# Kernel tuning notes

Hardware: AMD Instinct MI355X
Metric: run time of the kernel (lower is better)

## Reference

```python
import math
import jax, jax.numpy as jnp
import numpy as np

GROUPS = 32
EPS = 1e-5


def group_norm(x, w, b):
    # x: [B, C, H, W]
    B, C, H, W = x.shape
    xg = x.reshape(B, GROUPS, C // GROUPS, H, W)
    mean = xg.mean(axis=(2, 3, 4), keepdims=True)
    var = xg.var(axis=(2, 3, 4), keepdims=True)
    xg = (xg - mean) * jax.lax.rsqrt(var + EPS)
    x = xg.reshape(B, C, H, W)
    return x * w[None, :, None, None] + b[None, :, None, None]


def setup_inputs() -> dict:
    key = jax.random.key(0)
    ks = jax.random.split(key, 4)
    B, C, H, W = 16, 512, 32, 32
    x = jax.random.normal(ks[0], (B, C, H, W), dtype=jnp.float32)
    norm_w = jnp.ones((C,), dtype=jnp.float32)
    norm_b = jnp.zeros((C,), dtype=jnp.float32)
    qkv_w = jax.random.normal(ks[1], (3 * C, C), dtype=jnp.float32) / math.sqrt(C)
    qkv_b = jnp.zeros((3 * C,), dtype=jnp.float32)
    proj_w = jax.random.normal(ks[2], (C, C), dtype=jnp.float32) / math.sqrt(C)
    proj_b = jnp.zeros((C,), dtype=jnp.float32)
    return {"x": x, "norm_w": norm_w, "norm_b": norm_b,
            "qkv_w": qkv_w, "qkv_b": qkv_b,
            "proj_w": proj_w, "proj_b": proj_b}


def reference(x, norm_w, norm_b, qkv_w, qkv_b, proj_w, proj_b):
    B, C, H, W = x.shape
    xn = group_norm(x, norm_w, norm_b)
    # 1x1 conv == channel matmul: [B,3C,H,W]
    qkv = jnp.einsum('oc,bchw->bohw', qkv_w, xn) + qkv_b[None, :, None, None]
    q, k, v = jnp.split(qkv, 3, axis=1)
    q = q.reshape(B, C, H * W).transpose(0, 2, 1)  # [B, HW, C]
    k = k.reshape(B, C, H * W)                     # [B, C, HW]
    v = v.reshape(B, C, H * W).transpose(0, 2, 1)  # [B, HW, C]
    attn = jax.nn.softmax(jnp.einsum('bnc,bcm->bnm', q, k) / math.sqrt(C), axis=-1)
    h = jnp.einsum('bnm,bmc->bnc', attn, v)        # [B, HW, C]
    h = h.transpose(0, 2, 1).reshape(B, C, H, W)
    out = jnp.einsum('oc,bchw->bohw', proj_w, h) + proj_b[None, :, None, None]
    return out + x
```

## Files before the change

### kernel.cpp

```cpp
#include <hip/hip_runtime.h>

#define GLD16(gp, lp) __builtin_amdgcn_global_load_lds( \
    (const __attribute__((address_space(1))) void*)(gp), \
    (__attribute__((address_space(3))) void*)(lp), 16, 0, 0)

typedef __attribute__((ext_vector_type(8))) short bf16x8;
typedef __attribute__((ext_vector_type(4))) float f32x4;

__device__ __forceinline__ short f2bf(float f) {
    union { float f; unsigned u; } x; x.f = f;
    unsigned r = x.u + 0x7fffu + ((x.u >> 16) & 1u);
    return (short)(r >> 16);
}
__device__ __forceinline__ float bf2f(short s) {
    union { unsigned u; float f; } x;
    x.u = ((unsigned)(unsigned short)s) << 16;
    return x.f;
}
__device__ __forceinline__ int xcd_swz(int id, int n) {
    return (id & 7) * (n >> 3) + (id >> 3);
}

__global__ __launch_bounds__(256) void prep(
    const float* __restrict__ qkv_w, const float* __restrict__ proj_w,
    short* __restrict__ wq, short* __restrict__ wp,
    const float* __restrict__ x, float* __restrict__ mean, float* __restrict__ rstd)
{
    if (blockIdx.x < 1024) {
        int idx = blockIdx.x * 256 + threadIdx.x;
        const int NQ4 = (1536 * 512) / 4;
        float4 f; short4 s;
        if (idx < NQ4) {
            f = ((const float4*)qkv_w)[idx];
            s.x = f2bf(f.x); s.y = f2bf(f.y); s.z = f2bf(f.z); s.w = f2bf(f.w);
            ((short4*)wq)[idx] = s;
        } else {
            int j = idx - NQ4;
            f = ((const float4*)proj_w)[j];
            s.x = f2bf(f.x); s.y = f2bf(f.y); s.z = f2bf(f.z); s.w = f2bf(f.w);
            ((short4*)wp)[j] = s;
        }
    } else {
        int bg = blockIdx.x - 1024;
        const float4* p = (const float4*)(x + (size_t)bg * 16384);
        float s = 0.f, ss = 0.f;
        for (int i = threadIdx.x; i < 4096; i += 256) {
            float4 v = p[i];
            s  += v.x + v.y + v.z + v.w;
            ss += v.x * v.x + v.y * v.y + v.z * v.z + v.w * v.w;
        }
        #pragma unroll
        for (int o = 32; o > 0; o >>= 1) {
            s  += __shfl_down(s, o);
            ss += __shfl_down(ss, o);
        }
        __shared__ float ls[4], lss[4];
        int wave = threadIdx.x >> 6;
        if ((threadIdx.x & 63) == 0) { ls[wave] = s; lss[wave] = ss; }
        __syncthreads();
        if (threadIdx.x == 0) {
            s  = ls[0] + ls[1] + ls[2] + ls[3];
            ss = lss[0] + lss[1] + lss[2] + lss[3];
            float m = s * (1.f / 16384.f);
            float var = ss * (1.f / 16384.f) - m * m;
            mean[bg] = m;
            rstd[bg] = rsqrtf(var + 1e-5f);
        }
    }
}

__global__ __launch_bounds__(256) void gn_apply_t(
    const float* __restrict__ x, const float* __restrict__ w, const float* __restrict__ bb,
    const float* __restrict__ mean, const float* __restrict__ rstd,
    short* __restrict__ xnT)
{
    __shared__ short tile[64][65];
    int b = blockIdx.z, cblk = blockIdx.y, nblk = blockIdx.x;
    int t = threadIdx.x;
    int nl = t & 63;
    int cb = t >> 6;
    #pragma unroll
    for (int i = 0; i < 16; ++i) {
        int cl = cb * 16 + i;
        int cg = cblk * 64 + cl;
        int bgid = b * 32 + (cg >> 4);
        float sc = rstd[bgid] * w[cg];
        float sh = bb[cg] - mean[bgid] * sc;
        float xv = x[((size_t)(b * 512 + cg)) * 1024 + nblk * 64 + nl];
        tile[cl][nl] = f2bf(xv * sc + sh);
    }
    __syncthreads();
    int ng = t >> 4;
    int c4 = (t & 15) * 4;
    #pragma unroll
    for (int p = 0; p < 4; ++p) {
        int nl2 = p * 16 + ng;
        short4 sv;
        sv.x = tile[c4 + 0][nl2];
        sv.y = tile[c4 + 1][nl2];
        sv.z = tile[c4 + 2][nl2];
        sv.w = tile[c4 + 3][nl2];
        *(short4*)&xnT[((size_t)(b * 1024 + nblk * 64 + nl2)) * 512 + cblk * 64 + c4] = sv;
    }
}

template<int NT>
__device__ __forceinline__ void gemm256_8p(
    const short* __restrict__ A, const short* __restrict__ B,
    const int lda, const int ldb, short* lds, f32x4 acc[8][4])
{
    const int tid  = threadIdx.x;
    const int lane = tid & 63;
    const int wave = tid >> 6;
    const int wm = wave >> 2;
    const int wn = wave & 3;
    const int fr = lane & 15;
    const int fk = lane >> 4;

    const short* pa[2]; const short* pb[2]; int la[2], lb[2];
    #pragma unroll
    for (int i = 0; i < 2; ++i) {
        int cid = i * 512 + tid;
        int row = cid >> 2, sl = cid & 3;
        int csw = sl ^ ((row >> 1) & 3);
        pa[i] = A + (size_t)row * lda + csw * 8;
        pb[i] = B + (size_t)row * ldb + csw * 8;
        la[i] = cid * 8;
        lb[i] = 8192 + cid * 8;
    }

    #pragma unroll
    for (int i = 0; i < 2; ++i) GLD16(pa[i],      lds + la[i]);
    #pragma unroll
    for (int i = 0; i < 2; ++i) GLD16(pb[i],      lds + lb[i]);
    #pragma unroll
    for (int i = 0; i < 2; ++i) GLD16(pa[i] + 32, lds + 16384 + la[i]);
    #pragma unroll
    for (int i = 0; i < 2; ++i) GLD16(pb[i] + 32, lds + 16384 + lb[i]);
    asm volatile("s_waitcnt vmcnt(4)" ::: "memory");
    asm volatile("s_barrier" ::: "memory");

    const int arow0 = wm * 128 + fr;
    const int brow0 = wn * 64 + fr;

    int base = 0, sbase = 32768, kst = 64;
    for (int t = 0; t < NT; ++t) {
        const short* lA = lds + base;
        const short* lB = lds + base + 8192;
        const bool pre = (t + 2 < NT);

        if (pre) {
            GLD16(pa[0] + kst, lds + sbase + la[0]);
            GLD16(pa[1] + kst, lds + sbase + la[1]);
        }
        bf16x8 af[8], bf0[2];
        #pragma unroll
        for (int m = 0; m < 8; ++m) {
            int R = arow0 + m * 16;
            af[m] = *(const bf16x8*)&lA[R * 32 + ((fk ^ ((R >> 1) & 3)) << 3)];
        }
        #pragma unroll
        for (int n = 0; n < 2; ++n) {
            int R = brow0 + n * 16;
            bf0[n] = *(const bf16x8*)&lB[R * 32 + ((fk ^ ((R >> 1) & 3)) << 3)];
        }
        asm volatile("s_barrier" ::: "memory");
        __builtin_amdgcn_s_setprio(1);
        #pragma unroll
        for (int m = 0; m < 8; ++m)
            #pragma unroll
            for (int n = 0; n < 2; ++n)
                acc[m][n] = __builtin_amdgcn_mfma_f32_16x16x32_bf16(af[m], bf0[n], acc[m][n], 0, 0, 0);
        __builtin_amdgcn_s_setprio(0);

        if (pre) {
            GLD16(pb[0] + kst, lds + sbase + lb[0]);
            GLD16(pb[1] + kst, lds + sbase + lb[1]);
        }
        bf16x8 bf1[2];
        #pragma unroll
        for (int n = 0; n < 2; ++n) {
            int R = brow0 + (n + 2) * 16;
            bf1[n] = *(const bf16x8*)&lB[R * 32 + ((fk ^ ((R >> 1) & 3)) << 3)];
        }
        asm volatile("s_barrier" ::: "memory");
        __builtin_amdgcn_s_setprio(1);
        #pragma unroll
        for (int m = 0; m < 8; ++m)
            #pragma unroll
            for (int n = 0; n < 2; ++n)
                acc[m][n + 2] = __builtin_amdgcn_mfma_f32_16x16x32_bf16(af[m], bf1[n], acc[m][n + 2], 0, 0, 0);
        __builtin_amdgcn_s_setprio(0);

        if (pre)                 asm volatile("s_waitcnt vmcnt(4)" ::: "memory");
        else if (t + 1 < NT)     asm volatile("s_waitcnt vmcnt(0)" ::: "memory");
        asm volatile("s_barrier" ::: "memory");
        __builtin_amdgcn_sched_barrier(0);
        base  = (base  == 32768) ? 0 : base  + 16384;
        sbase = (sbase == 32768) ? 0 : sbase + 16384;
        kst += 32;
    }
}

template<int NT>
__device__ __forceinline__ void gemm128x256(
    const short* __restrict__ A, const short* __restrict__ B,
    const int lda, const int ldb, short* lds, f32x4 acc[4][4])
{
    const int tid  = threadIdx.x;
    const int lane = tid & 63;
    const int wave = tid >> 6;
    const int wm = wave >> 2;
    const int wn = wave & 3;
    const int fr = lane & 15;
    const int fk = lane >> 4;

    const short* pa; int la;
    {
        int row = tid >> 2, sl = tid & 3;
        int csw = sl ^ ((row >> 1) & 3);
        pa = A + (size_t)row * lda + csw * 8;
        la = tid * 8;
    }
    const short* pb[2]; int lb[2];
    #pragma unroll
    for (int i = 0; i < 2; ++i) {
        int cid = i * 512 + tid;
        int row = cid >> 2, sl = cid & 3;
        int csw = sl ^ ((row >> 1) & 3);
        pb[i] = B + (size_t)row * ldb + csw * 8;
        lb[i] = 4096 + cid * 8;
    }

    GLD16(pa, lds + la);
    #pragma unroll
    for (int i = 0; i < 2; ++i) GLD16(pb[i], lds + lb[i]);
    GLD16(pa + 32, lds + 12288 + la);
    #pragma unroll
    for (int i = 0; i < 2; ++i) GLD16(pb[i] + 32, lds + 12288 + lb[i]);
    asm volatile("s_waitcnt vmcnt(3)" ::: "memory");
    asm volatile("s_barrier" ::: "memory");

    const int arow0 = wm * 64 + fr;
    const int brow0 = wn * 64 + fr;

    int base = 0, sbase = 24576, kst = 64;
    for (int t = 0; t < NT; ++t) {
        const short* lA = lds + base;
        const short* lB = lds + base + 4096;
        const bool pre = (t + 2 < NT);

        if (pre) GLD16(pa + kst, lds + sbase + la);
        bf16x8 af[4], bf0[2];
        #pragma unroll
        for (int m = 0; m < 4; ++m) {
            int R = arow0 + m * 16;
            af[m] = *(const bf16x8*)&lA[R * 32 + ((fk ^ ((R >> 1) & 3)) << 3)];
        }
        #pragma unroll
        for (int n = 0; n < 2; ++n) {
            int R = brow0 + n * 16;
            bf0[n] = *(const bf16x8*)&lB[R * 32 + ((fk ^ ((R >> 1) & 3)) << 3)];
        }
        asm volatile("s_barrier" ::: "memory");
        __builtin_amdgcn_s_setprio(1);
        #pragma unroll
        for (int m = 0; m < 4; ++m)
            #pragma unroll
            for (int n = 0; n < 2; ++n)
                acc[m][n] = __builtin_amdgcn_mfma_f32_16x16x32_bf16(af[m], bf0[n], acc[m][n], 0, 0, 0);
        __builtin_amdgcn_s_setprio(0);

        if (pre) {
            GLD16(pb[0] + kst, lds + sbase + lb[0]);
            GLD16(pb[1] + kst, lds + sbase + lb[1]);
        }
        bf16x8 bf1[2];
        #pragma unroll
        for (int n = 0; n < 2; ++n) {
            int R = brow0 + (n + 2) * 16;
            bf1[n] = *(const bf16x8*)&lB[R * 32 + ((fk ^ ((R >> 1) & 3)) << 3)];
        }
        asm volatile("s_barrier" ::: "memory");
        __builtin_amdgcn_s_setprio(1);
        #pragma unroll
        for (int m = 0; m < 4; ++m)
            #pragma unroll
            for (int n = 0; n < 2; ++n)
                acc[m][n + 2] = __builtin_amdgcn_mfma_f32_16x16x32_bf16(af[m], bf1[n], acc[m][n + 2], 0, 0, 0);
        __builtin_amdgcn_s_setprio(0);

        if (pre)                 asm volatile("s_waitcnt vmcnt(3)" ::: "memory");
        else if (t + 1 < NT)     asm volatile("s_waitcnt vmcnt(0)" ::: "memory");
        asm volatile("s_barrier" ::: "memory");
        __builtin_amdgcn_sched_barrier(0);
        base  = (base  == 24576) ? 0 : base  + 12288;
        sbase = (sbase == 24576) ? 0 : sbase + 12288;
        kst += 32;
    }
}

#define EPI_IDX8() \
    const int lane = threadIdx.x & 63; \
    const int wave = threadIdx.x >> 6; \
    const int wm = wave >> 2; \
    const int wn = wave & 3; \
    const int fq = lane >> 4; \
    const int fcol = lane & 15;

__global__ __launch_bounds__(512, 2) void qkv_gemm(
    const short* __restrict__ wq, const float* __restrict__ qkv_b,
    const short* __restrict__ xnT,
    short* __restrict__ qT, short* __restrict__ kT, short* __restrict__ vv)
{
    __shared__ short lds[49152];
    int wg = xcd_swz(blockIdx.x, 384);
    const int bm = wg % 6, bn = wg / 6;
    const short* A  = wq + (size_t)bm * 256 * 512;
    const short* Bb = xnT + (size_t)bn * 256 * 512;
    f32x4 acc[8][4];
    #pragma unroll
    for (int m = 0; m < 8; ++m)
        #pragma unroll
        for (int n = 0; n < 4; ++n) acc[m][n] = (f32x4){0.f, 0.f, 0.f, 0.f};
    gemm256_8p<16>(A, Bb, 512, 512, lds, acc);

    EPI_IDX8();
    const int region = bm >> 1;
    const float qscale = 0.04419417382415922f;

    #pragma unroll
    for (int m = 0; m < 8; ++m) {
        int o0 = bm * 256 + wm * 128 + m * 16 + fq * 4;
        float4 bias = *(const float4*)&qkv_b[o0];
        float bb4[4] = {bias.x, bias.y, bias.z, bias.w};
        #pragma unroll
        for (int n = 0; n < 4; ++n) {
            int cf = bn * 256 + wn * 64 + n * 16 + fcol;
            int b = cf >> 10, col = cf & 1023;
            f32x4 a = acc[m][n];
            if (region == 0) {
                short4 sv;
                sv.x = f2bf((a[0] + bb4[0]) * qscale);
                sv.y = f2bf((a[1] + bb4[1]) * qscale);
                sv.z = f2bf((a[2] + bb4[2]) * qscale);
                sv.w = f2bf((a[3] + bb4[3]) * qscale);
                *(short4*)&qT[((size_t)(b * 1024 + col)) * 512 + o0] = sv;
            } else if (region == 1) {
                short4 sv;
                sv.x = f2bf(a[0] + bb4[0]);
                sv.y = f2bf(a[1] + bb4[1]);
                sv.z = f2bf(a[2] + bb4[2]);
                sv.w = f2bf(a[3] + bb4[3]);
                *(short4*)&kT[((size_t)(b * 1024 + col)) * 512 + (o0 - 512)] = sv;
            } else {
                #pragma unroll
                for (int r = 0; r < 4; ++r)
                    vv[((size_t)(b * 512 + (o0 - 1024 + r))) * 1024 + col] = f2bf(a[r] + bb4[r]);
            }
        }
    }
}

__global__ __launch_bounds__(512, 2) void s_gemm(
    const short* __restrict__ kT, const short* __restrict__ qT,
    short* __restrict__ S, float* __restrict__ rowsum)
{
    __shared__ short lds[49152];
    int wg = xcd_swz(blockIdx.x, 256);
    const int bn = wg & 3, bm = (wg >> 2) & 3, b = wg >> 4;
    const short* A  = kT + ((size_t)b * 1024 + bm * 256) * 512;
    const short* Bb = qT + ((size_t)b * 1024 + bn * 256) * 512;
    f32x4 acc[8][4];
    #pragma unroll
    for (int m = 0; m < 8; ++m)
        #pragma unroll
        for (int n = 0; n < 4; ++n) acc[m][n] = (f32x4){0.f, 0.f, 0.f, 0.f};
    gemm256_8p<16>(A, Bb, 512, 512, lds, acc);

    EPI_IDX8();
    float rs[4] = {0.f, 0.f, 0.f, 0.f};
    #pragma unroll
    for (int m = 0; m < 8; ++m) {
        int m0 = bm * 256 + wm * 128 + m * 16 + fq * 4;
        #pragma unroll
        for (int n = 0; n < 4; ++n) {
            int ncol = bn * 256 + wn * 64 + n * 16 + fcol;
            f32x4 a = acc[m][n];
            float e0 = __expf(fminf(a[0], 30.f));
            float e1 = __expf(fminf(a[1], 30.f));
            float e2 = __expf(fminf(a[2], 30.f));
            float e3 = __expf(fminf(a[3], 30.f));
            short4 sv;
            sv.x = f2bf(e0); sv.y = f2bf(e1); sv.z = f2bf(e2); sv.w = f2bf(e3);
            *(short4*)&S[((size_t)(b * 1024 + ncol)) * 1024 + m0] = sv;
            rs[n] += e0 + e1 + e2 + e3;
        }
    }
    #pragma unroll
    for (int n = 0; n < 4; ++n) {
        float v = rs[n];
        v += __shfl_xor(v, 16);
        v += __shfl_xor(v, 32);
        if (lane < 16) {
            int ncol = bn * 256 + wn * 64 + n * 16 + lane;
            atomicAdd(&rowsum[b * 1024 + ncol], v);
        }
    }
}

__global__ __launch_bounds__(512, 2) void pv_gemm(
    const short* __restrict__ vv, const short* __restrict__ P,
    const float* __restrict__ rowsum, short* __restrict__ h)
{
    __shared__ short lds[36864];
    int wg = xcd_swz(blockIdx.x, 256);
    const int bn = wg & 3, bm = (wg >> 2) & 3, b = wg >> 4;
    const short* A  = vv + ((size_t)b * 512 + bm * 128) * 1024;
    const short* Bb = P + ((size_t)b * 1024 + bn * 256) * 1024;
    f32x4 acc[4][4];
    #pragma unroll
    for (int m = 0; m < 4; ++m)
        #pragma unroll
        for (int n = 0; n < 4; ++n) acc[m][n] = (f32x4){0.f, 0.f, 0.f, 0.f};
    gemm128x256<32>(A, Bb, 1024, 1024, lds, acc);

    EPI_IDX8();
    float inv[4];
    #pragma unroll
    for (int n = 0; n < 4; ++n) {
        int ncol = bn * 256 + wn * 64 + n * 16 + fcol;
        inv[n] = 1.f / rowsum[b * 1024 + ncol];
    }
    #pragma unroll
    for (int m = 0; m < 4; ++m) {
        int c0 = bm * 128 + wm * 64 + m * 16 + fq * 4;
        #pragma unroll
        for (int n = 0; n < 4; ++n) {
            int ncol = bn * 256 + wn * 64 + n * 16 + fcol;
            f32x4 a = acc[m][n];
            short4 sv;
            sv.x = f2bf(a[0] * inv[n]); sv.y = f2bf(a[1] * inv[n]);
            sv.z = f2bf(a[2] * inv[n]); sv.w = f2bf(a[3] * inv[n]);
            *(short4*)&h[((size_t)(b * 1024 + ncol)) * 512 + c0] = sv;
        }
    }
}

__global__ __launch_bounds__(512, 2) void proj_gemm(
    const short* __restrict__ wp, const float* __restrict__ proj_b,
    const short* __restrict__ h, const float* __restrict__ x, float* __restrict__ out)
{
    __shared__ short lds[36864];
    int wg = xcd_swz(blockIdx.x, 256);
    const int bm = wg & 3, bn = wg >> 2;
    const short* A  = wp + (size_t)bm * 128 * 512;
    const short* Bb = h + (size_t)bn * 256 * 512;
    f32x4 acc[4][4];
    #pragma unroll
    for (int m = 0; m < 4; ++m)
        #pragma unroll
        for (int n = 0; n < 4; ++n) acc[m][n] = (f32x4){0.f, 0.f, 0.f, 0.f};
    gemm128x256<16>(A, Bb, 512, 512, lds, acc);

    EPI_IDX8();
    #pragma unroll
    for (int m = 0; m < 4; ++m) {
        int o0 = bm * 128 + wm * 64 + m * 16 + fq * 4;
        float4 pb = *(const float4*)&proj_b[o0];
        float pb4[4] = {pb.x, pb.y, pb.z, pb.w};
        #pragma unroll
        for (int n = 0; n < 4; ++n) {
            int cf = bn * 256 + wn * 64 + n * 16 + fcol;
            int b = cf >> 10, col = cf & 1023;
            f32x4 a = acc[m][n];
            #pragma unroll
            for (int r = 0; r < 4; ++r) {
                size_t idx = ((size_t)(b * 512 + o0 + r)) * 1024 + col;
                out[idx] = a[r] + pb4[r] + x[idx];
            }
        }
    }
}

extern "C" void kernel_launch(void* const* d_in, const int* in_sizes, int n_in,
                              void* d_out, int out_size, void* d_ws, size_t ws_size,
                              hipStream_t stream) {
    const float* x      = (const float*)d_in[0];
    const float* norm_w = (const float*)d_in[1];
    const float* norm_b = (const float*)d_in[2];
    const float* qkv_w  = (const float*)d_in[3];
    const float* qkv_b  = (const float*)d_in[4];
    const float* proj_w = (const float*)d_in[5];
    const float* proj_b = (const float*)d_in[6];
    float* out = (float*)d_out;

    char* ws = (char*)d_ws;
    size_t off = 0;
    auto alloc = [&](size_t bytes) {
        void* p = ws + off;
        off = (off + bytes + 255) & ~(size_t)255;
        return p;
    };
    float* mean   = (float*)alloc(512 * 4);
    float* rstd   = (float*)alloc(512 * 4);
    float* rowsum = (float*)alloc((size_t)16384 * 4);
    short* wq   = (short*)alloc((size_t)1536 * 512 * 2);
    short* wp   = (short*)alloc((size_t)512 * 512 * 2);
    short* xnT  = (short*)alloc((size_t)16 * 1024 * 512 * 2);
    short* qT   = (short*)alloc((size_t)16 * 1024 * 512 * 2);
    short* kT   = (short*)alloc((size_t)16 * 1024 * 512 * 2);
    short* vv   = (short*)alloc((size_t)16 * 512 * 1024 * 2);
    short* S    = (short*)alloc((size_t)16 * 1024 * 1024 * 2);
    short* h    = xnT;

    hipMemsetAsync(rowsum, 0, (size_t)16384 * 4, stream);
    prep<<<1536, 256, 0, stream>>>(qkv_w, proj_w, wq, wp, x, mean, rstd);
    gn_apply_t<<<dim3(16, 8, 16), 256, 0, stream>>>(x, norm_w, norm_b, mean, rstd, xnT);
    qkv_gemm<<<384, 512, 0, stream>>>(wq, qkv_b, xnT, qT, kT, vv);
    s_gemm<<<256, 512, 0, stream>>>(kT, qT, S, rowsum);
    pv_gemm<<<256, 512, 0, stream>>>(vv, S, rowsum, h);
    proj_gemm<<<256, 512, 0, stream>>>(wp, proj_b, h, x, out);
}
```

Before: 214.2 us.

## Switch 256x256 GEMM to double-buffered pipeline and fold rowsum memset into prep

```diff
diff --git a/kernel.cpp b/kernel.cpp
--- a/kernel.cpp
+++ b/kernel.cpp
@@ -24,7 +24,8 @@
 __global__ __launch_bounds__(256) void prep(
     const float* __restrict__ qkv_w, const float* __restrict__ proj_w,
     short* __restrict__ wq, short* __restrict__ wp,
-    const float* __restrict__ x, float* __restrict__ mean, float* __restrict__ rstd)
+    const float* __restrict__ x, float* __restrict__ mean, float* __restrict__ rstd,
+    float* __restrict__ rowsum)
 {
     if (blockIdx.x < 1024) {
         int idx = blockIdx.x * 256 + threadIdx.x;
@@ -42,6 +43,7 @@
         }
     } else {
         int bg = blockIdx.x - 1024;
+        if (threadIdx.x < 32) rowsum[bg * 32 + threadIdx.x] = 0.f;
         const float4* p = (const float4*)(x + (size_t)bg * 16384);
         float s = 0.f, ss = 0.f;
         for (int i = threadIdx.x; i < 4096; i += 256) {
@@ -105,7 +107,7 @@
 }
 
 template<int NT>
-__device__ __forceinline__ void gemm256_8p(
+__device__ __forceinline__ void gemm256_2b(
     const short* __restrict__ A, const short* __restrict__ B,
     const int lda, const int ldb, short* lds, f32x4 acc[8][4])
 {
@@ -130,75 +132,53 @@
     }
 
     #pragma unroll
-    for (int i = 0; i < 2; ++i) GLD16(pa[i],      lds + la[i]);
-    #pragma unroll
-    for (int i = 0; i < 2; ++i) GLD16(pb[i],      lds + lb[i]);
-    #pragma unroll
-    for (int i = 0; i < 2; ++i) GLD16(pa[i] + 32, lds + 16384 + la[i]);
-    #pragma unroll
-    for (int i = 0; i < 2; ++i) GLD16(pb[i] + 32, lds + 16384 + lb[i]);
-    asm volatile("s_waitcnt vmcnt(4)" ::: "memory");
+    for (int i = 0; i < 2; ++i) GLD16(pa[i], lds + la[i]);
+    #pragma unroll
+    for (int i = 0; i < 2; ++i) GLD16(pb[i], lds + lb[i]);
+    asm volatile("s_waitcnt vmcnt(0)" ::: "memory");
     asm volatile("s_barrier" ::: "memory");
 
     const int arow0 = wm * 128 + fr;
     const int brow0 = wn * 64 + fr;
 
-    int base = 0, sbase = 32768, kst = 64;
     for (int t = 0; t < NT; ++t) {
-        const short* lA = lds + base;
-        const short* lB = lds + base + 8192;
-        const bool pre = (t + 2 < NT);
+        const int cur = (t & 1) << 14;
+        const int nxt = 16384 - cur;
+        const bool pre = (t + 1 < NT);
+        const int kst = (t + 1) * 32;
+        const short* lA = lds + cur;
+        const short* lB = lds + cur + 8192;
 
         if (pre) {
-            GLD16(pa[0] + kst, lds + sbase + la[0]);
-            GLD16(pa[1] + kst, lds + sbase + la[1]);
-        }
-        bf16x8 af[8], bf0[2];
+            GLD16(pa[0] + kst, lds + nxt + la[0]);
+            GLD16(pa[1] + kst, lds + nxt + la[1]);
+            GLD16(pb[0] + kst, lds + nxt + lb[0]);
+            GLD16(pb[1] + kst, lds + nxt + lb[1]);
+        }
+        bf16x8 af[8], bfr[4];
         #pragma unroll
         for (int m = 0; m < 8; ++m) {
             int R = arow0 + m * 16;
             af[m] = *(const bf16x8*)&lA[R * 32 + ((fk ^ ((R >> 1) & 3)) << 3)];
         }
         #pragma unroll
-        for (int n = 0; n < 2; ++n) {
+        for (int n = 0; n < 4; ++n) {
             int R = brow0 + n * 16;
-            bf0[n] = *(const bf16x8*)&lB[R * 32 + ((fk ^ ((R >> 1) & 3)) << 3)];
-        }
-        asm volatile("s_barrier" ::: "memory");
+            bfr[n] = *(const bf16x8*)&lB[R * 32 + ((fk ^ ((R >> 1) & 3)) << 3)];
+        }
         __builtin_amdgcn_s_setprio(1);
         #pragma unroll
         for (int m = 0; m < 8; ++m)
             #pragma unroll
-            for (int n = 0; n < 2; ++n)
-                acc[m][n] = __builtin_amdgcn_mfma_f32_16x16x32_bf16(af[m], bf0[n], acc[m][n], 0, 0, 0);
+            for (int n = 0; n < 4; ++n)
+                acc[m][n] = __builtin_amdgcn_mfma_f32_16x16x32_bf16(af[m], bfr[n], acc[m][n], 0, 0, 0);
         __builtin_amdgcn_s_setprio(0);
 
         if (pre) {
-            GLD16(pb[0] + kst, lds + sbase + lb[0]);
-            GLD16(pb[1] + kst, lds + sbase + lb[1]);
-        }
-        bf16x8 bf1[2];
-        #pragma unroll
-        for (int n = 0; n < 2; ++n) {
-            int R = brow0 + (n + 2) * 16;
-            bf1[n] = *(const bf16x8*)&lB[R * 32 + ((fk ^ ((R >> 1) & 3)) << 3)];
-        }
-        asm volatile("s_barrier" ::: "memory");
-        __builtin_amdgcn_s_setprio(1);
-        #pragma unroll
-        for (int m = 0; m < 8; ++m)
-            #pragma unroll
-            for (int n = 0; n < 2; ++n)
-                acc[m][n + 2] = __builtin_amdgcn_mfma_f32_16x16x32_bf16(af[m], bf1[n], acc[m][n + 2], 0, 0, 0);
-        __builtin_amdgcn_s_setprio(0);
-
-        if (pre)                 asm volatile("s_waitcnt vmcnt(4)" ::: "memory");
-        else if (t + 1 < NT)     asm volatile("s_waitcnt vmcnt(0)" ::: "memory");
-        asm volatile("s_barrier" ::: "memory");
-        __builtin_amdgcn_sched_barrier(0);
-        base  = (base  == 32768) ? 0 : base  + 16384;
-        sbase = (sbase == 32768) ? 0 : sbase + 16384;
-        kst += 32;
+            asm volatile("s_waitcnt vmcnt(0)" ::: "memory");
+            asm volatile("s_barrier" ::: "memory");
+            __builtin_amdgcn_sched_barrier(0);
+        }
     }
 }
 
@@ -313,7 +293,7 @@
     const short* __restrict__ xnT,
     short* __restrict__ qT, short* __restrict__ kT, short* __restrict__ vv)
 {
-    __shared__ short lds[49152];
+    __shared__ short lds[32768];
     int wg = xcd_swz(blockIdx.x, 384);
     const int bm = wg % 6, bn = wg / 6;
     const short* A  = wq + (size_t)bm * 256 * 512;
@@ -323,7 +303,7 @@
     for (int m = 0; m < 8; ++m)
         #pragma unroll
         for (int n = 0; n < 4; ++n) acc[m][n] = (f32x4){0.f, 0.f, 0.f, 0.f};
-    gemm256_8p<16>(A, Bb, 512, 512, lds, acc);
+    gemm256_2b<16>(A, Bb, 512, 512, lds, acc);
 
     EPI_IDX8();
     const int region = bm >> 1;
@@ -366,7 +346,7 @@
     const short* __restrict__ kT, const short* __restrict__ qT,
     short* __restrict__ S, float* __restrict__ rowsum)
 {
-    __shared__ short lds[49152];
+    __shared__ short lds[32768];
     int wg = xcd_swz(blockIdx.x, 256);
     const int bn = wg & 3, bm = (wg >> 2) & 3, b = wg >> 4;
     const short* A  = kT + ((size_t)b * 1024 + bm * 256) * 512;
@@ -376,7 +356,7 @@
     for (int m = 0; m < 8; ++m)
         #pragma unroll
         for (int n = 0; n < 4; ++n) acc[m][n] = (f32x4){0.f, 0.f, 0.f, 0.f};
-    gemm256_8p<16>(A, Bb, 512, 512, lds, acc);
+    gemm256_2b<16>(A, Bb, 512, 512, lds, acc);
 
     EPI_IDX8();
     float rs[4] = {0.f, 0.f, 0.f, 0.f};
@@ -514,8 +494,7 @@
     short* S    = (short*)alloc((size_t)16 * 1024 * 1024 * 2);
     short* h    = xnT;
 
-    hipMemsetAsync(rowsum, 0, (size_t)16384 * 4, stream);
-    prep<<<1536, 256, 0, stream>>>(qkv_w, proj_w, wq, wp, x, mean, rstd);
+    prep<<<1536, 256, 0, stream>>>(qkv_w, proj_w, wq, wp, x, mean, rstd, rowsum);
     gn_apply_t<<<dim3(16, 8, 16), 256, 0, stream>>>(x, norm_w, norm_b, mean, rstd, xnT);
     qkv_gemm<<<384, 512, 0, stream>>>(wq, qkv_b, xnT, qT, kT, vv);
     s_gemm<<<256, 512, 0, stream>>>(kT, qT, S, rowsum);
```

Result: slower. 224.8 us (+5.0%).
